# Kernel optimization log

Hardware: AMD Instinct MI355X
Metric: run time of the kernel (lower is better)

## Reference

```python
import jax, jax.numpy as jnp
import numpy as np

B, N, DIN, DOUT = 32, 1024, 256, 256


def setup_inputs() -> dict:
    key = jax.random.key(0)
    ks = jax.random.split(key, 7)
    s = 1.0 / np.sqrt(DIN)
    return {
        "x": jax.random.normal(ks[0], (B, N, DIN), dtype=jnp.float32),
        "Wq": jax.random.uniform(ks[1], (DOUT, DIN), minval=-s, maxval=s, dtype=jnp.float32),
        "bq": jax.random.uniform(ks[2], (DOUT,), minval=-s, maxval=s, dtype=jnp.float32),
        "Wk": jax.random.uniform(ks[3], (DOUT, DIN), minval=-s, maxval=s, dtype=jnp.float32),
        "bk": jax.random.uniform(ks[4], (DOUT,), minval=-s, maxval=s, dtype=jnp.float32),
        "Wv": jax.random.uniform(ks[5], (DOUT, DIN), minval=-s, maxval=s, dtype=jnp.float32),
        "bv": jax.random.uniform(ks[6], (DOUT,), minval=-s, maxval=s, dtype=jnp.float32),
    }


def reference(x, Wq, bq, Wk, bk, Wv, bv):
    # q, k, v: (B, N, Dout)
    q = jnp.einsum("bnd,od->bno", x, Wq) + bq
    k = jnp.einsum("bnd,od->bno", x, Wk) + bk
    v = jnp.einsum("bnd,od->bno", x, Wv) + bv
    # logits: (B, N, N) = q @ k^T per batch
    logits = jnp.einsum("bnd,bmd->bnm", q, k)
    # NOTE: softmax over the BATCH dim (axis=0), as in the original module
    attn = jax.nn.softmax(logits, axis=0)
    out = jnp.einsum("bnm,bmd->bnd", attn, v)  # (B, N, Dout)
    return out
```

## Files before the change

### kernel.cpp

```cpp
#include <hip/hip_runtime.h>

typedef __bf16 bf16x8 __attribute__((ext_vector_type(8)));
typedef __bf16 bf16x4 __attribute__((ext_vector_type(4)));
typedef float  f32x4  __attribute__((ext_vector_type(4)));

#define BM 128
#define BN 128
#define BK 64

__device__ __forceinline__ void g2l16(const void* g, void* l) {
    __builtin_amdgcn_global_load_lds((const __attribute__((address_space(1))) void*)g,
                                     (__attribute__((address_space(3))) void*)l, 16, 0, 0);
}

template<int EPI, int SWZ>
__global__ __launch_bounds__(256)
void gemm_nt(const __bf16* __restrict__ A, const __bf16* __restrict__ B,
             void* __restrict__ Cv, const float* __restrict__ bias,
             int lda, int ldb, int ldc, int K,
             long sA, long sB, long sC)
{
    __shared__ __align__(16) __bf16 As[BM * BK];
    __shared__ __align__(16) __bf16 Bs[BN * BK];

    const int tid  = threadIdx.x;
    const int w    = tid >> 6;
    const int lane = tid & 63;
    const int quad = lane >> 4;
    const int l16  = lane & 15;
    const int wm   = w & 1;
    const int wn   = w >> 1;

    int m0, n0, z;
    if constexpr (SWZ == 1) {
        const int id = blockIdx.x;
        const int x  = id & 7, s = id >> 3;
        z = x + ((s >> 6) << 3);
        const int t = s & 63;
        m0 = (t & 7) * BM;
        n0 = (t >> 3) * BN;
    } else {
        m0 = blockIdx.x * BM;
        n0 = blockIdx.y * BN;
        z  = blockIdx.z;
    }

    const __bf16* Ab = A + (size_t)z * sA;
    const __bf16* Bb = B + (size_t)z * sB;

    const int srow = (w << 3) + (lane >> 3);
    const int scol = ((lane & 7) ^ (lane >> 3)) << 3;
    char* ldsA = (char*)As + (size_t)w * 1024;
    char* ldsB = (char*)Bs + (size_t)w * 1024;

    const __bf16* Ag = Ab + (size_t)(m0 + srow) * lda + scol;
    const __bf16* Bg = Bb + (size_t)(n0 + srow) * ldb + scol;

    f32x4 acc[4][4] = {};

    for (int k0 = 0; k0 < K; k0 += BK) {
        __syncthreads();
        #pragma unroll
        for (int c = 0; c < 4; c++)
            g2l16(Ag + (size_t)(c * 32) * lda + k0, ldsA + c * 4096);
        #pragma unroll
        for (int c = 0; c < 4; c++)
            g2l16(Bg + (size_t)(c * 32) * ldb + k0, ldsB + c * 4096);
        __syncthreads();

        #pragma unroll
        for (int kk = 0; kk < BK; kk += 32) {
            const int ub = kk >> 3;
            bf16x8 a[4], b[4];
            #pragma unroll
            for (int mt = 0; mt < 4; mt++) {
                const int row = wm * 64 + mt * 16 + l16;
                const int cp  = ((quad + ub) ^ (row & 7)) << 3;
                a[mt] = *(const bf16x8*)&As[row * BK + cp];
            }
            #pragma unroll
            for (int nt = 0; nt < 4; nt++) {
                const int row = wn * 64 + nt * 16 + l16;
                const int cp  = ((quad + ub) ^ (row & 7)) << 3;
                b[nt] = *(const bf16x8*)&Bs[row * BK + cp];
            }
            #pragma unroll
            for (int mt = 0; mt < 4; mt++)
                #pragma unroll
                for (int nt = 0; nt < 4; nt++)
                    acc[mt][nt] = __builtin_amdgcn_mfma_f32_16x16x32_bf16(
                        a[mt], b[nt], acc[mt][nt], 0, 0, 0);
        }
    }

    #pragma unroll
    for (int mt = 0; mt < 4; mt++) {
        const int mb = m0 + wm * 64 + mt * 16 + quad * 4;
        #pragma unroll
        for (int nt = 0; nt < 4; nt++) {
            const int n = n0 + wn * 64 + nt * 16 + l16;
            if constexpr (EPI == 2) {
                __bf16* C = (__bf16*)Cv + (size_t)z * sC;
                #pragma unroll
                for (int r = 0; r < 4; r++)
                    C[(size_t)(mb + r) * ldc + n] = (__bf16)__expf(acc[mt][nt][r]);
            } else {
                const float bn = bias[z * 256 + n];
                if (z < 2) {
                    __bf16* C = (__bf16*)Cv + (size_t)z * sC;
                    #pragma unroll
                    for (int r = 0; r < 4; r++)
                        C[(size_t)(mb + r) * ldc + n] = (__bf16)(acc[mt][nt][r] + bn);
                } else {
                    __bf16* C = (__bf16*)Cv + 2 * sC;
                    const int bidx = mb >> 10, mloc = mb & 1023;
                    bf16x4 pk;
                    #pragma unroll
                    for (int r = 0; r < 4; r++) pk[r] = (__bf16)(acc[mt][nt][r] + bn);
                    *(bf16x4*)(C + (size_t)bidx * 262144 + (size_t)n * 1024 + mloc) = pk;
                }
            }
        }
    }
}

__global__ __launch_bounds__(256)
void gemm_pv(const __bf16* __restrict__ E, const __bf16* __restrict__ vT,
             float* __restrict__ out)
{
    __shared__ __align__(16) __bf16 As[128 * 64];
    __shared__ __align__(16) __bf16 Bs[64 * 64];

    const int tid  = threadIdx.x;
    const int w    = tid >> 6;
    const int lane = tid & 63;
    const int quad = lane >> 4;
    const int l16  = lane & 15;
    const int wm   = w & 1;
    const int wn   = w >> 1;

    const int id = blockIdx.x;
    const int x  = id & 7, s = id >> 3;
    const int z  = x + ((s >> 5) << 3);
    const int t  = s & 31;
    const int m0 = (t & 7) * 128;
    const int n0 = (t >> 3) * 64;

    const __bf16* Eb = E  + (size_t)z * 1048576;
    const __bf16* Vb = vT + (size_t)z * 262144;
    float*        Ob = out + (size_t)z * 262144;

    const int srow = (w << 3) + (lane >> 3);
    const int scol = ((lane & 7) ^ (lane >> 3)) << 3;
    char* ldsA = (char*)As + (size_t)w * 1024;
    char* ldsB = (char*)Bs + (size_t)w * 1024;

    const __bf16* Ag = Eb + (size_t)(m0 + srow) * 1024 + scol;
    const __bf16* Bg = Vb + (size_t)(n0 + srow) * 1024 + scol;

    f32x4 acc[4][2] = {};

    for (int k0 = 0; k0 < 1024; k0 += BK) {
        __syncthreads();
        #pragma unroll
        for (int c = 0; c < 4; c++)
            g2l16(Ag + (size_t)(c * 32) * 1024 + k0, ldsA + c * 4096);
        #pragma unroll
        for (int c = 0; c < 2; c++)
            g2l16(Bg + (size_t)(c * 32) * 1024 + k0, ldsB + c * 4096);
        __syncthreads();

        #pragma unroll
        for (int kk = 0; kk < BK; kk += 32) {
            const int ub = kk >> 3;
            bf16x8 a[4], b[2];
            #pragma unroll
            for (int mt = 0; mt < 4; mt++) {
                const int row = wm * 64 + mt * 16 + l16;
                const int cp  = ((quad + ub) ^ (row & 7)) << 3;
                a[mt] = *(const bf16x8*)&As[row * BK + cp];
            }
            #pragma unroll
            for (int nt = 0; nt < 2; nt++) {
                const int row = wn * 32 + nt * 16 + l16;
                const int cp  = ((quad + ub) ^ (row & 7)) << 3;
                b[nt] = *(const bf16x8*)&Bs[row * BK + cp];
            }
            #pragma unroll
            for (int mt = 0; mt < 4; mt++)
                #pragma unroll
                for (int nt = 0; nt < 2; nt++)
                    acc[mt][nt] = __builtin_amdgcn_mfma_f32_16x16x32_bf16(
                        a[mt], b[nt], acc[mt][nt], 0, 0, 0);
        }
    }

    #pragma unroll
    for (int mt = 0; mt < 4; mt++) {
        const int mb = m0 + wm * 64 + mt * 16 + quad * 4;
        #pragma unroll
        for (int nt = 0; nt < 2; nt++) {
            const int n = n0 + wn * 32 + nt * 16 + l16;
            #pragma unroll
            for (int r = 0; r < 4; r++)
                Ob[(size_t)(mb + r) * 256 + n] = acc[mt][nt][r];
        }
    }
}

__global__ __launch_bounds__(256)
void cvt_all(const float* __restrict__ x,
             const float* __restrict__ Wq, const float* __restrict__ Wk,
             const float* __restrict__ Wv,
             const float* __restrict__ bq, const float* __restrict__ bk,
             const float* __restrict__ bv,
             __bf16* __restrict__ xb, __bf16* __restrict__ Wqb,
             float* __restrict__ bpack)
{
    const int i = blockIdx.x * 256 + threadIdx.x;
    if (i < 1073152) {
        const float* s; __bf16* d; int off;
        if (i < 1048576)      { s = x;  d = xb;            off = i; }
        else if (i < 1056768) { s = Wq; d = Wqb;           off = i - 1048576; }
        else if (i < 1064960) { s = Wk; d = Wqb + 131072;  off = i - 1056768; }
        else                  { s = Wv; d = Wqb + 262144;  off = i - 1064960; }
        const float4* s4 = (const float4*)s;
        const float4 f0 = s4[off * 2], f1 = s4[off * 2 + 1];
        bf16x8 o;
        o[0] = (__bf16)f0.x; o[1] = (__bf16)f0.y; o[2] = (__bf16)f0.z; o[3] = (__bf16)f0.w;
        o[4] = (__bf16)f1.x; o[5] = (__bf16)f1.y; o[6] = (__bf16)f1.z; o[7] = (__bf16)f1.w;
        ((bf16x8*)d)[off] = o;
    } else if (i < 1073344) {
        const int j = i - 1073152;
        const int sel = j >> 6, jj = j & 63;
        const float* s = sel == 0 ? bq : (sel == 1 ? bk : bv);
        ((float4*)bpack)[j] = ((const float4*)s)[jj];
    }
}

__global__ __launch_bounds__(256)
void softmax_norm(__bf16* __restrict__ E)
{
    const size_t p = (size_t)blockIdx.x * 256 + threadIdx.x;
    bf16x8* E8 = (bf16x8*)E;
    bf16x8 e[32];
    #pragma unroll
    for (int b = 0; b < 32; b++) e[b] = E8[(size_t)b * 131072 + p];
    float s[8] = {0.f, 0.f, 0.f, 0.f, 0.f, 0.f, 0.f, 0.f};
    #pragma unroll
    for (int b = 0; b < 32; b++)
        #pragma unroll
        for (int j = 0; j < 8; j++) s[j] += (float)e[b][j];
    float rs[8];
    #pragma unroll
    for (int j = 0; j < 8; j++) rs[j] = __builtin_amdgcn_rcpf(s[j]);
    #pragma unroll
    for (int b = 0; b < 32; b++) {
        bf16x8 o = e[b];
        #pragma unroll
        for (int j = 0; j < 8; j++) o[j] = (__bf16)((float)o[j] * rs[j]);
        E8[(size_t)b * 131072 + p] = o;
    }
}

extern "C" void kernel_launch(void* const* d_in, const int* in_sizes, int n_in,
                              void* d_out, int out_size, void* d_ws, size_t ws_size,
                              hipStream_t stream)
{
    const float* x  = (const float*)d_in[0];
    const float* Wq = (const float*)d_in[1];
    const float* bq = (const float*)d_in[2];
    const float* Wk = (const float*)d_in[3];
    const float* bk = (const float*)d_in[4];
    const float* Wv = (const float*)d_in[5];
    const float* bv = (const float*)d_in[6];
    float* out = (float*)d_out;

    char* ws = (char*)d_ws;
    __bf16* xb    = (__bf16*)(ws);
    __bf16* qkv   = (__bf16*)(ws + (16u << 20));
    __bf16* E     = (__bf16*)(ws + (64u << 20));
    __bf16* Wqb   = (__bf16*)(ws + (128u << 20));
    float*  bpack = (float*) (ws + (128u << 20) + (3u << 18));

    cvt_all<<<4194, 256, 0, stream>>>(x, Wq, Wk, Wv, bq, bk, bv, xb, Wqb, bpack);

    gemm_nt<4, 0><<<dim3(256, 2, 3), 256, 0, stream>>>(xb, Wqb, qkv, bpack,
                                                       256, 256, 256, 256,
                                                       0, 131072, 8388608);

    gemm_nt<2, 1><<<2048, 256, 0, stream>>>(qkv, qkv + 8388608, E, nullptr,
                                            256, 256, 1024, 256,
                                            262144, 262144, 1048576);

    softmax_norm<<<512, 256, 0, stream>>>(E);

    gemm_pv<<<1024, 256, 0, stream>>>(E, qkv + 2 * 8388608, out);
}
```

Baseline: 192.3 us.

## Fuse fp32-to-bf16 conversion into projection GEMM and stage exp logits through LDS

```diff
diff --git a/kernel.cpp b/kernel.cpp
--- a/kernel.cpp
+++ b/kernel.cpp
@@ -4,8 +4,6 @@
 typedef __bf16 bf16x4 __attribute__((ext_vector_type(4)));
 typedef float  f32x4  __attribute__((ext_vector_type(4)));
 
-#define BM 128
-#define BN 128
 #define BK 64
 
 __device__ __forceinline__ void g2l16(const void* g, void* l) {
@@ -13,15 +11,24 @@
                                      (__attribute__((address_space(3))) void*)l, 16, 0, 0);
 }
 
-template<int EPI, int SWZ>
+__device__ __forceinline__ bf16x8 cvt8(const float* p) {
+    const float4 f0 = *(const float4*)p, f1 = *(const float4*)(p + 4);
+    bf16x8 o;
+    o[0] = (__bf16)f0.x; o[1] = (__bf16)f0.y; o[2] = (__bf16)f0.z; o[3] = (__bf16)f0.w;
+    o[4] = (__bf16)f1.x; o[5] = (__bf16)f1.y; o[6] = (__bf16)f1.z; o[7] = (__bf16)f1.w;
+    return o;
+}
+
 __global__ __launch_bounds__(256)
-void gemm_nt(const __bf16* __restrict__ A, const __bf16* __restrict__ B,
-             void* __restrict__ Cv, const float* __restrict__ bias,
-             int lda, int ldb, int ldc, int K,
-             long sA, long sB, long sC)
-{
-    __shared__ __align__(16) __bf16 As[BM * BK];
-    __shared__ __align__(16) __bf16 Bs[BN * BK];
+void gemm_proj(const float* __restrict__ x,
+               const float* __restrict__ Wq, const float* __restrict__ Wk,
+               const float* __restrict__ Wv,
+               const float* __restrict__ bq, const float* __restrict__ bk,
+               const float* __restrict__ bv,
+               __bf16* __restrict__ qkv, __bf16* __restrict__ vT)
+{
+    __shared__ __align__(16) __bf16 As[128 * 64];
+    __shared__ __align__(16) __bf16 Bs[128 * 64];
 
     const int tid  = threadIdx.x;
     const int w    = tid >> 6;
@@ -31,41 +38,32 @@
     const int wm   = w & 1;
     const int wn   = w >> 1;
 
-    int m0, n0, z;
-    if constexpr (SWZ == 1) {
-        const int id = blockIdx.x;
-        const int x  = id & 7, s = id >> 3;
-        z = x + ((s >> 6) << 3);
-        const int t = s & 63;
-        m0 = (t & 7) * BM;
-        n0 = (t >> 3) * BN;
-    } else {
-        m0 = blockIdx.x * BM;
-        n0 = blockIdx.y * BN;
-        z  = blockIdx.z;
-    }
-
-    const __bf16* Ab = A + (size_t)z * sA;
-    const __bf16* Bb = B + (size_t)z * sB;
-
-    const int srow = (w << 3) + (lane >> 3);
-    const int scol = ((lane & 7) ^ (lane >> 3)) << 3;
-    char* ldsA = (char*)As + (size_t)w * 1024;
-    char* ldsB = (char*)Bs + (size_t)w * 1024;
-
-    const __bf16* Ag = Ab + (size_t)(m0 + srow) * lda + scol;
-    const __bf16* Bg = Bb + (size_t)(n0 + srow) * ldb + scol;
+    const int m0 = blockIdx.x * 128;
+    const int n0 = blockIdx.y * 128;
+    const int z  = blockIdx.z;
+
+    const float* W  = z == 0 ? Wq : (z == 1 ? Wk : Wv);
+    const float* bb = z == 0 ? bq : (z == 1 ? bk : bv);
+
+    const int row  = tid >> 1;
+    const int half = tid & 1;
+    const float* Ag = x + (size_t)(m0 + row) * 256 + half * 32;
+    const float* Bg = W + (size_t)(n0 + row) * 256 + half * 32;
+    __bf16* Adst = As + row * 64;
+    __bf16* Bdst = Bs + row * 64;
 
     f32x4 acc[4][4] = {};
 
-    for (int k0 = 0; k0 < K; k0 += BK) {
-        __syncthreads();
-        #pragma unroll
-        for (int c = 0; c < 4; c++)
-            g2l16(Ag + (size_t)(c * 32) * lda + k0, ldsA + c * 4096);
-        #pragma unroll
-        for (int c = 0; c < 4; c++)
-            g2l16(Bg + (size_t)(c * 32) * ldb + k0, ldsB + c * 4096);
+    for (int k0 = 0; k0 < 256; k0 += BK) {
+        __syncthreads();
+        #pragma unroll
+        for (int s = 0; s < 4; s++) {
+            const int u = half * 4 + s;
+            bf16x8 pa = cvt8(Ag + k0 + s * 8);
+            bf16x8 pb = cvt8(Bg + k0 + s * 8);
+            *(bf16x8*)(Adst + ((u ^ (row & 7)) << 3)) = pa;
+            *(bf16x8*)(Bdst + ((u ^ (row & 7)) << 3)) = pb;
+        }
         __syncthreads();
 
         #pragma unroll
@@ -74,15 +72,13 @@
             bf16x8 a[4], b[4];
             #pragma unroll
             for (int mt = 0; mt < 4; mt++) {
-                const int row = wm * 64 + mt * 16 + l16;
-                const int cp  = ((quad + ub) ^ (row & 7)) << 3;
-                a[mt] = *(const bf16x8*)&As[row * BK + cp];
+                const int rr = wm * 64 + mt * 16 + l16;
+                a[mt] = *(const bf16x8*)&As[rr * 64 + (((quad + ub) ^ (rr & 7)) << 3)];
             }
             #pragma unroll
             for (int nt = 0; nt < 4; nt++) {
-                const int row = wn * 64 + nt * 16 + l16;
-                const int cp  = ((quad + ub) ^ (row & 7)) << 3;
-                b[nt] = *(const bf16x8*)&Bs[row * BK + cp];
+                const int rr = wn * 64 + nt * 16 + l16;
+                b[nt] = *(const bf16x8*)&Bs[rr * 64 + (((quad + ub) ^ (rr & 7)) << 3)];
             }
             #pragma unroll
             for (int mt = 0; mt < 4; mt++)
@@ -99,37 +95,30 @@
         #pragma unroll
         for (int nt = 0; nt < 4; nt++) {
             const int n = n0 + wn * 64 + nt * 16 + l16;
-            if constexpr (EPI == 2) {
-                __bf16* C = (__bf16*)Cv + (size_t)z * sC;
+            const float bn = bb[n];
+            if (z < 2) {
+                __bf16* C = qkv + (size_t)z * 8388608;
                 #pragma unroll
                 for (int r = 0; r < 4; r++)
-                    C[(size_t)(mb + r) * ldc + n] = (__bf16)__expf(acc[mt][nt][r]);
+                    C[(size_t)(mb + r) * 256 + n] = (__bf16)(acc[mt][nt][r] + bn);
             } else {
-                const float bn = bias[z * 256 + n];
-                if (z < 2) {
-                    __bf16* C = (__bf16*)Cv + (size_t)z * sC;
-                    #pragma unroll
-                    for (int r = 0; r < 4; r++)
-                        C[(size_t)(mb + r) * ldc + n] = (__bf16)(acc[mt][nt][r] + bn);
-                } else {
-                    __bf16* C = (__bf16*)Cv + 2 * sC;
-                    const int bidx = mb >> 10, mloc = mb & 1023;
-                    bf16x4 pk;
-                    #pragma unroll
-                    for (int r = 0; r < 4; r++) pk[r] = (__bf16)(acc[mt][nt][r] + bn);
-                    *(bf16x4*)(C + (size_t)bidx * 262144 + (size_t)n * 1024 + mloc) = pk;
-                }
+                const int bidx = mb >> 10, mloc = mb & 1023;
+                bf16x4 pk;
+                #pragma unroll
+                for (int r = 0; r < 4; r++) pk[r] = (__bf16)(acc[mt][nt][r] + bn);
+                *(bf16x4*)(vT + (size_t)bidx * 262144 + (size_t)n * 1024 + mloc) = pk;
             }
         }
     }
 }
 
 __global__ __launch_bounds__(256)
-void gemm_pv(const __bf16* __restrict__ E, const __bf16* __restrict__ vT,
-             float* __restrict__ out)
-{
-    __shared__ __align__(16) __bf16 As[128 * 64];
-    __shared__ __align__(16) __bf16 Bs[64 * 64];
+void gemm_logits(const __bf16* __restrict__ qb, const __bf16* __restrict__ kb,
+                 __bf16* __restrict__ E)
+{
+    __shared__ __align__(16) char smem[33792];
+    __bf16* As = (__bf16*)smem;
+    __bf16* Bs = (__bf16*)(smem + 16384);
 
     const int tid  = threadIdx.x;
     const int w    = tid >> 6;
@@ -140,20 +129,134 @@
     const int wn   = w >> 1;
 
     const int id = blockIdx.x;
-    const int x  = id & 7, s = id >> 3;
-    const int z  = x + ((s >> 5) << 3);
-    const int t  = s & 31;
+    const int x8 = id & 7, s = id >> 3;
+    const int z  = x8 + ((s >> 6) << 3);
+    const int t  = s & 63;
     const int m0 = (t & 7) * 128;
-    const int n0 = (t >> 3) * 64;
-
-    const __bf16* Eb = E  + (size_t)z * 1048576;
-    const __bf16* Vb = vT + (size_t)z * 262144;
-    float*        Ob = out + (size_t)z * 262144;
+    const int n0 = (t >> 3) * 128;
+
+    const __bf16* Ab = qb + (size_t)z * 262144;
+    const __bf16* Bb = kb + (size_t)z * 262144;
 
     const int srow = (w << 3) + (lane >> 3);
     const int scol = ((lane & 7) ^ (lane >> 3)) << 3;
     char* ldsA = (char*)As + (size_t)w * 1024;
     char* ldsB = (char*)Bs + (size_t)w * 1024;
+    const __bf16* Ag = Ab + (size_t)(m0 + srow) * 256 + scol;
+    const __bf16* Bg = Bb + (size_t)(n0 + srow) * 256 + scol;
+
+    f32x4 acc[4][4] = {};
+
+    for (int k0 = 0; k0 < 256; k0 += BK) {
+        __syncthreads();
+        #pragma unroll
+        for (int c = 0; c < 4; c++)
+            g2l16(Ag + (size_t)(c * 32) * 256 + k0, ldsA + c * 4096);
+        #pragma unroll
+        for (int c = 0; c < 4; c++)
+            g2l16(Bg + (size_t)(c * 32) * 256 + k0, ldsB + c * 4096);
+        __syncthreads();
+
+        #pragma unroll
+        for (int kk = 0; kk < BK; kk += 32) {
+            const int ub = kk >> 3;
+            bf16x8 a[4], b[4];
+            #pragma unroll
+            for (int mt = 0; mt < 4; mt++) {
+                const int rr = wm * 64 + mt * 16 + l16;
+                a[mt] = *(const bf16x8*)&As[rr * 64 + (((quad + ub) ^ (rr & 7)) << 3)];
+            }
+            #pragma unroll
+            for (int nt = 0; nt < 4; nt++) {
+                const int rr = wn * 64 + nt * 16 + l16;
+                b[nt] = *(const bf16x8*)&Bs[rr * 64 + (((quad + ub) ^ (rr & 7)) << 3)];
+            }
+            #pragma unroll
+            for (int mt = 0; mt < 4; mt++)
+                #pragma unroll
+                for (int nt = 0; nt < 4; nt++)
+                    acc[mt][nt] = __builtin_amdgcn_mfma_f32_16x16x32_bf16(
+                        a[mt], b[nt], acc[mt][nt], 0, 0, 0);
+        }
+    }
+
+    __syncthreads();
+    __bf16* eb = (__bf16*)smem;
+    #pragma unroll
+    for (int mt = 0; mt < 4; mt++) {
+        const int rb = wm * 64 + mt * 16 + quad * 4;
+        #pragma unroll
+        for (int nt = 0; nt < 4; nt++) {
+            const int c = wn * 64 + nt * 16 + l16;
+            #pragma unroll
+            for (int r = 0; r < 4; r++)
+                eb[(rb + r) * 132 + c] = (__bf16)__expf(acc[mt][nt][r]);
+        }
+    }
+    __syncthreads();
+    const int row = tid >> 1, seg = tid & 1;
+    __bf16* dst = E + (size_t)z * 1048576 + (size_t)(m0 + row) * 1024 + n0 + seg * 64;
+    const __bf16* src = eb + row * 132 + seg * 64;
+    #pragma unroll
+    for (int u = 0; u < 8; u++)
+        *(bf16x8*)(dst + u * 8) = *(const bf16x8*)(src + u * 8);
+}
+
+__global__ __launch_bounds__(256)
+void softmax_norm(__bf16* __restrict__ E)
+{
+    const size_t p = (size_t)blockIdx.x * 256 + threadIdx.x;
+    bf16x8* E8 = (bf16x8*)E;
+    bf16x8 e[32];
+    #pragma unroll
+    for (int b = 0; b < 32; b++) e[b] = E8[(size_t)b * 131072 + p];
+    float sm[8] = {0.f, 0.f, 0.f, 0.f, 0.f, 0.f, 0.f, 0.f};
+    #pragma unroll
+    for (int b = 0; b < 32; b++)
+        #pragma unroll
+        for (int j = 0; j < 8; j++) sm[j] += (float)e[b][j];
+    float rs[8];
+    #pragma unroll
+    for (int j = 0; j < 8; j++) rs[j] = __builtin_amdgcn_rcpf(sm[j]);
+    #pragma unroll
+    for (int b = 0; b < 32; b++) {
+        bf16x8 o = e[b];
+        #pragma unroll
+        for (int j = 0; j < 8; j++) o[j] = (__bf16)((float)o[j] * rs[j]);
+        E8[(size_t)b * 131072 + p] = o;
+    }
+}
+
+__global__ __launch_bounds__(256)
+void gemm_pv(const __bf16* __restrict__ E, const __bf16* __restrict__ vT,
+             float* __restrict__ out)
+{
+    __shared__ __align__(16) __bf16 As[128 * 64];
+    __shared__ __align__(16) __bf16 Bs[64 * 64];
+
+    const int tid  = threadIdx.x;
+    const int w    = tid >> 6;
+    const int lane = tid & 63;
+    const int quad = lane >> 4;
+    const int l16  = lane & 15;
+    const int wm   = w & 1;
+    const int wn   = w >> 1;
+
+    const int id = blockIdx.x;
+    const int x8 = id & 7, s = id >> 3;
+    const int z  = x8 + ((s >> 5) << 3);
+    const int t  = s & 31;
+    const int m0 = (t & 7) * 128;
+    const int n0 = (t >> 3) * 64;
+
+    const __bf16* Eb = E  + (size_t)z * 1048576;
+    const __bf16* Vb = vT + (size_t)z * 262144;
+    float*        Ob = out + (size_t)z * 262144;
+
+    const int srow = (w << 3) + (lane >> 3);
+    const int scol = ((lane & 7) ^ (lane >> 3)) << 3;
+    char* ldsA = (char*)As + (size_t)w * 1024;
+    char* ldsB = (char*)Bs + (size_t)w * 1024;
 
     const __bf16* Ag = Eb + (size_t)(m0 + srow) * 1024 + scol;
     const __bf16* Bg = Vb + (size_t)(n0 + srow) * 1024 + scol;
@@ -176,15 +279,13 @@
             bf16x8 a[4], b[2];
             #pragma unroll
             for (int mt = 0; mt < 4; mt++) {
-                const int row = wm * 64 + mt * 16 + l16;
-                const int cp  = ((quad + ub) ^ (row & 7)) << 3;
-                a[mt] = *(const bf16x8*)&As[row * BK + cp];
+                const int rr = wm * 64 + mt * 16 + l16;
+                a[mt] = *(const bf16x8*)&As[rr * 64 + (((quad + ub) ^ (rr & 7)) << 3)];
             }
             #pragma unroll
             for (int nt = 0; nt < 2; nt++) {
-                const int row = wn * 32 + nt * 16 + l16;
-                const int cp  = ((quad + ub) ^ (row & 7)) << 3;
-                b[nt] = *(const bf16x8*)&Bs[row * BK + cp];
+                const int rr = wn * 32 + nt * 16 + l16;
+                b[nt] = *(const bf16x8*)&Bs[rr * 64 + (((quad + ub) ^ (rr & 7)) << 3)];
             }
             #pragma unroll
             for (int mt = 0; mt < 4; mt++)
@@ -205,61 +306,6 @@
             for (int r = 0; r < 4; r++)
                 Ob[(size_t)(mb + r) * 256 + n] = acc[mt][nt][r];
         }
-    }
-}
-
-__global__ __launch_bounds__(256)
-void cvt_all(const float* __restrict__ x,
-             const float* __restrict__ Wq, const float* __restrict__ Wk,
-             const float* __restrict__ Wv,
-             const float* __restrict__ bq, const float* __restrict__ bk,
-             const float* __restrict__ bv,
-             __bf16* __restrict__ xb, __bf16* __restrict__ Wqb,
-             float* __restrict__ bpack)
-{
-    const int i = blockIdx.x * 256 + threadIdx.x;
-    if (i < 1073152) {
-        const float* s; __bf16* d; int off;
-        if (i < 1048576)      { s = x;  d = xb;            off = i; }
-        else if (i < 1056768) { s = Wq; d = Wqb;           off = i - 1048576; }
-        else if (i < 1064960) { s = Wk; d = Wqb + 131072;  off = i - 1056768; }
-        else                  { s = Wv; d = Wqb + 262144;  off = i - 1064960; }
-        const float4* s4 = (const float4*)s;
-        const float4 f0 = s4[off * 2], f1 = s4[off * 2 + 1];
-        bf16x8 o;
-        o[0] = (__bf16)f0.x; o[1] = (__bf16)f0.y; o[2] = (__bf16)f0.z; o[3] = (__bf16)f0.w;
-        o[4] = (__bf16)f1.x; o[5] = (__bf16)f1.y; o[6] = (__bf16)f1.z; o[7] = (__bf16)f1.w;
-        ((bf16x8*)d)[off] = o;
-    } else if (i < 1073344) {
-        const int j = i - 1073152;
-        const int sel = j >> 6, jj = j & 63;
-        const float* s = sel == 0 ? bq : (sel == 1 ? bk : bv);
-        ((float4*)bpack)[j] = ((const float4*)s)[jj];
-    }
-}
-
-__global__ __launch_bounds__(256)
-void softmax_norm(__bf16* __restrict__ E)
-{
-    const size_t p = (size_t)blockIdx.x * 256 + threadIdx.x;
-    bf16x8* E8 = (bf16x8*)E;
-    bf16x8 e[32];
-    #pragma unroll
-    for (int b = 0; b < 32; b++) e[b] = E8[(size_t)b * 131072 + p];
-    float s[8] = {0.f, 0.f, 0.f, 0.f, 0.f, 0.f, 0.f, 0.f};
-    #pragma unroll
-    for (int b = 0; b < 32; b++)
-        #pragma unroll
-        for (int j = 0; j < 8; j++) s[j] += (float)e[b][j];
-    float rs[8];
-    #pragma unroll
-    for (int j = 0; j < 8; j++) rs[j] = __builtin_amdgcn_rcpf(s[j]);
-    #pragma unroll
-    for (int b = 0; b < 32; b++) {
-        bf16x8 o = e[b];
-        #pragma unroll
-        for (int j = 0; j < 8; j++) o[j] = (__bf16)((float)o[j] * rs[j]);
-        E8[(size_t)b * 131072 + p] = o;
     }
 }
 
@@ -277,23 +323,16 @@
     float* out = (float*)d_out;
 
     char* ws = (char*)d_ws;
-    __bf16* xb    = (__bf16*)(ws);
-    __bf16* qkv   = (__bf16*)(ws + (16u << 20));
-    __bf16* E     = (__bf16*)(ws + (64u << 20));
-    __bf16* Wqb   = (__bf16*)(ws + (128u << 20));
-    float*  bpack = (float*) (ws + (128u << 20) + (3u << 18));
-
-    cvt_all<<<4194, 256, 0, stream>>>(x, Wq, Wk, Wv, bq, bk, bv, xb, Wqb, bpack);
-
-    gemm_nt<4, 0><<<dim3(256, 2, 3), 256, 0, stream>>>(xb, Wqb, qkv, bpack,
-                                                       256, 256, 256, 256,
-                                                       0, 131072, 8388608);
-
-    gemm_nt<2, 1><<<2048, 256, 0, stream>>>(qkv, qkv + 8388608, E, nullptr,
-                                            256, 256, 1024, 256,
-                                            262144, 262144, 1048576);
+    __bf16* qkv = (__bf16*)(ws + (16u << 20));
+    __bf16* vT  = (__bf16*)(ws + (48u << 20));
+    __bf16* E   = (__bf16*)(ws + (64u << 20));
+
+    gemm_proj<<<dim3(256, 2, 3), 256, 0, stream>>>(x, Wq, Wk, Wv, bq, bk, bv,
+                                                   qkv, vT);
+
+    gemm_logits<<<2048, 256, 0, stream>>>(qkv, qkv + 8388608, E);
 
     softmax_norm<<<512, 256, 0, stream>>>(E);
 
-    gemm_pv<<<1024, 256, 0, stream>>>(E, qkv + 2 * 8388608, out);
-}
+    gemm_pv<<<1024, 256, 0, stream>>>(E, vT, out);
+}
```

New measurement: 231.4 us. +20.3%, slower.
